# Kernel optimization log

Hardware: AMD Instinct MI355X
Metric: run time of the kernel (lower is better)

Reference implementation:

```python
import jax, jax.numpy as jnp
import numpy as np


def _init_boxes(C, F, max_h, max_w, seed=0):
    # Mirrors BoxConv2d.reset_parameters: random centers/sizes in pixel units,
    # then normalized by max_input_h / max_input_w (reparametrize).
    rng = np.random.default_rng(seed)
    min_h = min_w = 2.0
    ch = rng.uniform(-max_h * 2 / 4.8 + 1 + min_h / 2, max_h * 2 / 4.8 - 1 - min_h / 2, (C, F))
    cw = rng.uniform(-max_w * 2 / 4.8 + 1 + min_w / 2, max_w * 2 / 4.8 - 1 - min_w / 2, (C, F))
    hh = 2.0 * rng.uniform(min_h / 2, np.minimum(max_h - 1 - ch, ch + max_h - 1))
    ww = 2.0 * rng.uniform(min_w / 2, np.minimum(max_w - 1 - cw, cw + max_w - 1))
    x_min = (ch - hh / 2) / max_h
    x_max = (ch + hh / 2) / max_h
    y_min = (cw - ww / 2) / max_w
    y_max = (cw + ww / 2) / max_w
    return [jnp.asarray(a, jnp.float32) for a in (x_min, x_max, y_min, y_max)]


def setup_inputs() -> dict:
    key = jax.random.key(0)
    B, C, F, H, W = 8, 32, 8, 128, 128
    x = jax.random.normal(key, (B, C, H, W), dtype=jnp.float32)
    x_min, x_max, y_min, y_max = _init_boxes(C, F, H, W)
    return {"input": x, "x_min": x_min, "x_max": x_max, "y_min": y_min,
            "y_max": y_max, "max_input_h": H, "max_input_w": W}


def reference(input, x_min, x_max, y_min, y_max, max_input_h, max_input_w):
    # Exact box convolution: out[b, c*F+f, h, w] = continuous-area sum of
    # input[b, c] over rectangle [h+xm, h+xM+1] x [w+ym, w+yM+1], computed
    # by bilinear interpolation of the integral image (fractional corners).
    B, C, H, W = input.shape
    F = x_min.shape[1]
    dt = input.dtype
    # stored params are normalized; recover pixel-unit coordinates
    xm = x_min * max_input_h
    xM = x_max * max_input_h
    ym = y_min * max_input_w
    yM = y_max * max_input_w
    # integral image: I[b,c,i,j] = sum of input over rows<i, cols<j  -> [B,C,H+1,W+1]
    I = jnp.pad(jnp.cumsum(jnp.cumsum(input, axis=2), axis=3),
                ((0, 0), (0, 0), (1, 0), (1, 0)))
    h = jnp.arange(H, dtype=dt)
    w = jnp.arange(W, dtype=dt)
    Hf = jnp.asarray(H, dt)
    Wf = jnp.asarray(W, dt)
    u0 = jnp.clip(h[None, None, :] + xm[:, :, None], 0.0, Hf)        # [C,F,H]
    u1 = jnp.clip(h[None, None, :] + xM[:, :, None] + 1.0, 0.0, Hf)  # [C,F,H]
    v0 = jnp.clip(w[None, None, :] + ym[:, :, None], 0.0, Wf)        # [C,F,W]
    v1 = jnp.clip(w[None, None, :] + yM[:, :, None] + 1.0, 0.0, Wf)  # [C,F,W]

    Ie = I[:, :, None, :, :]  # [B,C,1,H+1,W+1]

    def row_interp(u):  # u: [C,F,H] -> [B,C,F,H,W+1]
        i0 = jnp.clip(jnp.floor(u), 0.0, Hf - 1.0)
        a = (u - i0)[None, :, :, :, None]
        i0 = i0.astype(jnp.int32)[None, :, :, :, None]
        g0 = jnp.take_along_axis(Ie, i0, axis=3)
        g1 = jnp.take_along_axis(Ie, i0 + 1, axis=3)
        return (1.0 - a) * g0 + a * g1

    # row-differenced, row-interpolated integral image
    Drow = row_interp(u1) - row_interp(u0)  # [B,C,F,H,W+1]

    def col_interp(v):  # v: [C,F,W] -> [B,C,F,H,W]
        j0 = jnp.clip(jnp.floor(v), 0.0, Wf - 1.0)
        b = (v - j0)[None, :, :, None, :]
        j0 = j0.astype(jnp.int32)[None, :, :, None, :]
        g0 = jnp.take_along_axis(Drow, j0, axis=4)
        g1 = jnp.take_along_axis(Drow, j0 + 1, axis=4)
        return (1.0 - b) * g0 + b * g1

    out = col_interp(v1) - col_interp(v0)  # [B,C,F,H,W]
    return out.reshape(B, C * F, H, W)
```

## Files before the change

### kernel.cpp

```cpp
#include <hip/hip_runtime.h>


__global__ __launch_bounds__(256, 2)
void boxconv_kernel(const float* __restrict__ in,
                    const float* __restrict__ x_min,
                    const float* __restrict__ x_max,
                    const float* __restrict__ y_min,
                    const float* __restrict__ y_max,
                    float* __restrict__ out)
{
    constexpr int H = 128, W = 128, C = 32, F = 8;
    constexpr int STRIDE = 132;
    constexpr int NROW = 129;

    __shared__ float I[NROW * STRIDE];
    __shared__ float Dbuf[4][STRIDE];

    const int tid  = threadIdx.x;
    const int lane = tid & 63;
    const int wid  = tid >> 6;

    const int bc   = blockIdx.x >> 1;
    const int half = blockIdx.x & 1;
    const int b    = bc >> 5;
    const int c    = bc & 31;

    {
        float4 z = make_float4(0.f, 0.f, 0.f, 0.f);
        float4* I4 = (float4*)I;
        for (int idx = tid; idx < (NROW * STRIDE) / 4; idx += 256) I4[idx] = z;
    }
    __syncthreads();

    const float* img = in + (size_t)bc * (H * W);
    if (tid < H) {
        const int r = tid;
        const float4* row4 = (const float4*)(img + r * W);
        float* Irow = I + (r + 1) * STRIDE + 1;
        float acc = 0.f;
        #pragma unroll 8
        for (int w4 = 0; w4 < W / 4; ++w4) {
            float4 v = row4[w4];
            float s0 = acc + v.x;
            float s1 = s0 + v.y;
            float s2 = s1 + v.z;
            float s3 = s2 + v.w;
            Irow[w4 * 4 + 0] = s0;
            Irow[w4 * 4 + 1] = s1;
            Irow[w4 * 4 + 2] = s2;
            Irow[w4 * 4 + 3] = s3;
            acc = s3;
        }
    }
    __syncthreads();

    if (tid < W) {
        const int cc = tid + 1;
        float acc = 0.f;
        for (int chunk = 0; chunk < 4; ++chunk) {
            const int r0 = 1 + chunk * 32;
            float v[32];
            #pragma unroll
            for (int i = 0; i < 32; ++i) v[i] = I[(r0 + i) * STRIDE + cc];
            #pragma unroll
            for (int i = 0; i < 32; ++i) { acc += v[i]; v[i] = acc; }
            #pragma unroll
            for (int i = 0; i < 32; ++i) I[(r0 + i) * STRIDE + cc] = v[i];
        }
    }
    __syncthreads();

    float* outbc = out + ((size_t)b * (C * F) + (size_t)c * F) * (H * W);

    for (int fi = 0; fi < 4; ++fi) {
        const int f = half * 4 + fi;
        const float xm = x_min[c * F + f] * 128.f;
        const float xM = x_max[c * F + f] * 128.f;
        const float ym = y_min[c * F + f] * 128.f;
        const float yM = y_max[c * F + f] * 128.f;

        int   j0[2], j1[2];
        float b0v[2], b1v[2], cb0[2], cb1[2];
        #pragma unroll
        for (int k = 0; k < 2; ++k) {
            const float wf = (float)(lane + 64 * k);
            const float v0 = fminf(fmaxf(wf + ym, 0.f), 128.f);
            const float v1 = fminf(fmaxf(wf + yM + 1.f, 0.f), 128.f);
            const float j0f = fminf(floorf(v0), 127.f);
            const float j1f = fminf(floorf(v1), 127.f);
            j0[k] = (int)j0f;  j1[k] = (int)j1f;
            b0v[k] = v0 - j0f; b1v[k] = v1 - j1f;
            cb0[k] = 1.f - b0v[k]; cb1[k] = 1.f - b1v[k];
        }

        float* Dw = Dbuf[wid];
        float* outf = outbc + (size_t)f * (H * W);

        for (int h = wid; h < H; h += 4) {
            const float hf = (float)h;
            const float u0 = fminf(fmaxf(hf + xm, 0.f), 128.f);
            const float u1 = fminf(fmaxf(hf + xM + 1.f, 0.f), 128.f);
            const float i0f = fminf(floorf(u0), 127.f);
            const float i1f = fminf(floorf(u1), 127.f);
            const int   i0  = (int)i0f, i1 = (int)i1f;
            const float a0 = u0 - i0f, a1 = u1 - i1f;
            const float ca0 = 1.f - a0, ca1 = 1.f - a1;

            if (lane < 33) {
                const int wp = lane * 4;
                const float4 q0  = *(const float4*)(I + i0 * STRIDE + wp);
                const float4 q0b = *(const float4*)(I + (i0 + 1) * STRIDE + wp);
                const float4 q1  = *(const float4*)(I + i1 * STRIDE + wp);
                const float4 q1b = *(const float4*)(I + (i1 + 1) * STRIDE + wp);
                float4 d;
                d.x = ca1 * q1.x + a1 * q1b.x - ca0 * q0.x - a0 * q0b.x;
                d.y = ca1 * q1.y + a1 * q1b.y - ca0 * q0.y - a0 * q0b.y;
                d.z = ca1 * q1.z + a1 * q1b.z - ca0 * q0.z - a0 * q0b.z;
                d.w = ca1 * q1.w + a1 * q1b.w - ca0 * q0.w - a0 * q0b.w;
                *(float4*)(Dw + wp) = d;
            }

            #pragma unroll
            for (int k = 0; k < 2; ++k) {
                const float Dj0  = Dw[j0[k]];
                const float Dj0p = Dw[j0[k] + 1];
                const float Dj1  = Dw[j1[k]];
                const float Dj1p = Dw[j1[k] + 1];
                outf[h * W + lane + 64 * k] =
                    cb1[k] * Dj1 + b1v[k] * Dj1p - cb0[k] * Dj0 - b0v[k] * Dj0p;
            }
        }
    }
}

extern "C" void kernel_launch(void* const* d_in, const int* in_sizes, int n_in,
                              void* d_out, int out_size, void* d_ws, size_t ws_size,
                              hipStream_t stream) {
    const float* in    = (const float*)d_in[0];
    const float* x_min = (const float*)d_in[1];
    const float* x_max = (const float*)d_in[2];
    const float* y_min = (const float*)d_in[3];
    const float* y_max = (const float*)d_in[4];
    float* outp = (float*)d_out;

    boxconv_kernel<<<dim3(8 * 32 * 2), dim3(256), 0, stream>>>(
        in, x_min, x_max, y_min, y_max, outp);
}
```

Baseline: 166.7 us.

## Process all filters per image in one 1024-thread block, two rows per wave

Each block now handles a full (batch, channel) image with 16 waves, each wave covering one filter and half the rows. This removes the duplicated integral-image construction across two blocks and zeroes only the buffer borders. The row-interpolation step now uses all 64 lanes to produce two rows at a time instead of leaving half the wave idle. The trade-off is fewer, larger blocks, with most threads idle during the scan phases and heavy LDS use per block.

```diff
diff --git a/kernel.cpp b/kernel.cpp
--- a/kernel.cpp
+++ b/kernel.cpp
@@ -1,7 +1,7 @@
 #include <hip/hip_runtime.h>
 
 
-__global__ __launch_bounds__(256, 2)
+__global__ __launch_bounds__(1024, 4)
 void boxconv_kernel(const float* __restrict__ in,
                     const float* __restrict__ x_min,
                     const float* __restrict__ x_max,
@@ -14,22 +14,16 @@
     constexpr int NROW = 129;
 
     __shared__ float I[NROW * STRIDE];
-    __shared__ float Dbuf[4][STRIDE];
+    __shared__ float Dbuf[16][2 * STRIDE];
 
     const int tid  = threadIdx.x;
     const int lane = tid & 63;
     const int wid  = tid >> 6;
-
-    const int bc   = blockIdx.x >> 1;
-    const int half = blockIdx.x & 1;
-    const int b    = bc >> 5;
+    const int bc   = blockIdx.x;
     const int c    = bc & 31;
 
-    {
-        float4 z = make_float4(0.f, 0.f, 0.f, 0.f);
-        float4* I4 = (float4*)I;
-        for (int idx = tid; idx < (NROW * STRIDE) / 4; idx += 256) I4[idx] = z;
-    }
+    if (tid < NROW)                    I[tid * STRIDE] = 0.f;
+    else if (tid >= 256 && tid < 256 + STRIDE - 1) I[tid - 255] = 0.f;
     __syncthreads();
 
     const float* img = in + (size_t)bc * (H * W);
@@ -70,63 +64,73 @@
     }
     __syncthreads();
 
-    float* outbc = out + ((size_t)b * (C * F) + (size_t)c * F) * (H * W);
+    const int f     = wid >> 1;
+    const int hbase = (wid & 1) * 64;
 
-    for (int fi = 0; fi < 4; ++fi) {
-        const int f = half * 4 + fi;
-        const float xm = x_min[c * F + f] * 128.f;
-        const float xM = x_max[c * F + f] * 128.f;
-        const float ym = y_min[c * F + f] * 128.f;
-        const float yM = y_max[c * F + f] * 128.f;
+    const float xm = x_min[c * F + f] * 128.f;
+    const float xM = x_max[c * F + f] * 128.f;
+    const float ym = y_min[c * F + f] * 128.f;
+    const float yM = y_max[c * F + f] * 128.f;
 
-        int   j0[2], j1[2];
-        float b0v[2], b1v[2], cb0[2], cb1[2];
-        #pragma unroll
-        for (int k = 0; k < 2; ++k) {
-            const float wf = (float)(lane + 64 * k);
-            const float v0 = fminf(fmaxf(wf + ym, 0.f), 128.f);
-            const float v1 = fminf(fmaxf(wf + yM + 1.f, 0.f), 128.f);
-            const float j0f = fminf(floorf(v0), 127.f);
-            const float j1f = fminf(floorf(v1), 127.f);
-            j0[k] = (int)j0f;  j1[k] = (int)j1f;
-            b0v[k] = v0 - j0f; b1v[k] = v1 - j1f;
-            cb0[k] = 1.f - b0v[k]; cb1[k] = 1.f - b1v[k];
+    int   j0[2], j1[2];
+    float b0v[2], b1v[2], cb0[2], cb1[2];
+    #pragma unroll
+    for (int k = 0; k < 2; ++k) {
+        const float wf = (float)(lane + 64 * k);
+        const float v0 = fminf(fmaxf(wf + ym, 0.f), 128.f);
+        const float v1 = fminf(fmaxf(wf + yM + 1.f, 0.f), 128.f);
+        const float j0f = fminf(floorf(v0), 127.f);
+        const float j1f = fminf(floorf(v1), 127.f);
+        j0[k] = (int)j0f;  j1[k] = (int)j1f;
+        b0v[k] = v0 - j0f; b1v[k] = v1 - j1f;
+        cb0[k] = 1.f - b0v[k]; cb1[k] = 1.f - b1v[k];
+    }
+
+    const int rsub = lane >> 5;
+    const int wp   = (lane & 31) * 4;
+    float* Dw = Dbuf[wid];
+    float* outf = out + ((size_t)bc * F + f) * (H * W);
+
+    for (int it = 0; it < 32; ++it) {
+        const int h = hbase + it * 2;
+
+        const float hf = (float)(h + rsub);
+        const float u0 = fminf(fmaxf(hf + xm, 0.f), 128.f);
+        const float u1 = fminf(fmaxf(hf + xM + 1.f, 0.f), 128.f);
+        const float i0f = fminf(floorf(u0), 127.f);
+        const float i1f = fminf(floorf(u1), 127.f);
+        const int   i0  = (int)i0f, i1 = (int)i1f;
+        const float a0 = u0 - i0f, a1 = u1 - i1f;
+        const float ca0 = 1.f - a0, ca1 = 1.f - a1;
+
+        const float* p0 = I + i0 * STRIDE;
+        const float* p1 = I + i1 * STRIDE;
+        const float4 q0  = *(const float4*)(p0 + wp);
+        const float4 q0b = *(const float4*)(p0 + STRIDE + wp);
+        const float4 q1  = *(const float4*)(p1 + wp);
+        const float4 q1b = *(const float4*)(p1 + STRIDE + wp);
+        float4 d;
+        d.x = ca1 * q1.x + a1 * q1b.x - ca0 * q0.x - a0 * q0b.x;
+        d.y = ca1 * q1.y + a1 * q1b.y - ca0 * q0.y - a0 * q0b.y;
+        d.z = ca1 * q1.z + a1 * q1b.z - ca0 * q0.z - a0 * q0b.z;
+        d.w = ca1 * q1.w + a1 * q1b.w - ca0 * q0.w - a0 * q0b.w;
+        *(float4*)(Dw + rsub * STRIDE + wp) = d;
+        if ((lane & 31) == 31) {
+            Dw[rsub * STRIDE + 128] =
+                ca1 * p1[128] + a1 * p1[STRIDE + 128]
+              - ca0 * p0[128] - a0 * p0[STRIDE + 128];
         }
 
-        float* Dw = Dbuf[wid];
-        float* outf = outbc + (size_t)f * (H * W);
-
-        for (int h = wid; h < H; h += 4) {
-            const float hf = (float)h;
-            const float u0 = fminf(fmaxf(hf + xm, 0.f), 128.f);
-            const float u1 = fminf(fmaxf(hf + xM + 1.f, 0.f), 128.f);
-            const float i0f = fminf(floorf(u0), 127.f);
-            const float i1f = fminf(floorf(u1), 127.f);
-            const int   i0  = (int)i0f, i1 = (int)i1f;
-            const float a0 = u0 - i0f, a1 = u1 - i1f;
-            const float ca0 = 1.f - a0, ca1 = 1.f - a1;
-
-            if (lane < 33) {
-                const int wp = lane * 4;
-                const float4 q0  = *(const float4*)(I + i0 * STRIDE + wp);
-                const float4 q0b = *(const float4*)(I + (i0 + 1) * STRIDE + wp);
-                const float4 q1  = *(const float4*)(I + i1 * STRIDE + wp);
-                const float4 q1b = *(const float4*)(I + (i1 + 1) * STRIDE + wp);
-                float4 d;
-                d.x = ca1 * q1.x + a1 * q1b.x - ca0 * q0.x - a0 * q0b.x;
-                d.y = ca1 * q1.y + a1 * q1b.y - ca0 * q0.y - a0 * q0b.y;
-                d.z = ca1 * q1.z + a1 * q1b.z - ca0 * q0.z - a0 * q0b.z;
-                d.w = ca1 * q1.w + a1 * q1b.w - ca0 * q0.w - a0 * q0b.w;
-                *(float4*)(Dw + wp) = d;
-            }
-
+        #pragma unroll
+        for (int rr = 0; rr < 2; ++rr) {
+            const float* Dr = Dw + rr * STRIDE;
             #pragma unroll
             for (int k = 0; k < 2; ++k) {
-                const float Dj0  = Dw[j0[k]];
-                const float Dj0p = Dw[j0[k] + 1];
-                const float Dj1  = Dw[j1[k]];
-                const float Dj1p = Dw[j1[k] + 1];
-                outf[h * W + lane + 64 * k] =
+                const float Dj0  = Dr[j0[k]];
+                const float Dj0p = Dr[j0[k] + 1];
+                const float Dj1  = Dr[j1[k]];
+                const float Dj1p = Dr[j1[k] + 1];
+                outf[(h + rr) * W + lane + 64 * k] =
                     cb1[k] * Dj1 + b1v[k] * Dj1p - cb0[k] * Dj0 - b0v[k] * Dj0p;
             }
         }
@@ -143,6 +147,6 @@
     const float* y_max = (const float*)d_in[4];
     float* outp = (float*)d_out;
 
-    boxconv_kernel<<<dim3(8 * 32 * 2), dim3(256), 0, stream>>>(
+    boxconv_kernel<<<dim3(8 * 32), dim3(1024), 0, stream>>>(
         in, x_min, x_max, y_min, y_max, outp);
 }
```

New measurement: 157.5 us. 5.5% less time.
